# Optimization experiments

Measured on AMD Instinct MI355X. Metric: run time of the kernel, lower is better.

The kernel has to match this reference:

```python
import jax, jax.numpy as jnp
import numpy as np

N_NODES = 50000
N_EDGES = 500000
HEADS = 4
OUT_CH = 64
POS_DIM = 16
IN_CH = 256
DIVERSITY_WEIGHT = 0.1
NEG_SLOPE = 0.2


def setup_inputs() -> dict:
    key = jax.random.key(0)
    k = jax.random.split(key, 6)
    x = jax.random.normal(k[0], (N_NODES, IN_CH + POS_DIM), dtype=jnp.float32)
    # edges with no self-loops by construction (col = row + nonzero offset mod N)
    row = jax.random.randint(k[1], (N_EDGES,), 0, N_NODES)
    off = jax.random.randint(k[2], (N_EDGES,), 1, N_NODES)
    col = (row + off) % N_NODES
    edge_index = jnp.stack([row, col]).astype(jnp.int64)
    lin_w = jax.random.normal(k[3], (HEADS * OUT_CH, IN_CH), dtype=jnp.float32) * (1.0 / np.sqrt(IN_CH))
    att = jax.random.normal(k[4], (1, HEADS, 2 * OUT_CH), dtype=jnp.float32) * 0.1
    pos_att = jax.random.normal(k[5], (1, HEADS, 2 * POS_DIM), dtype=jnp.float32) * 0.1
    bias = jnp.zeros((HEADS * OUT_CH,), dtype=jnp.float32)
    return {"x": x, "edge_index": edge_index, "lin_w": lin_w, "att": att,
            "pos_att": pos_att, "bias": bias}


def _forward(x, edge_index, lin_w, att, pos_att, bias):
    N = x.shape[0]
    H, C = HEADS, OUT_CH
    pos = x[:, -POS_DIM:]              # [N, P]
    content_feat = x[:, :-POS_DIM]     # [N, IN_CH]
    content = (content_feat @ lin_w.T).reshape(N, H, C)  # [N, H, C]

    # add self loops (input edges contain none)
    sl = jnp.arange(N)
    row = jnp.concatenate([edge_index[0], sl])  # [E+N]
    col = jnp.concatenate([edge_index[1], sl])

    # cat([x_i, x_j]) * att summed == per-node split logits, gathered per edge
    a_src = jnp.einsum('nhc,hc->nh', content, att[0, :, :C])   # [N, H]
    a_dst = jnp.einsum('nhc,hc->nh', content, att[0, :, C:])
    p_src = pos @ pos_att[0, :, :POS_DIM].T                    # [N, H]
    p_dst = pos @ pos_att[0, :, POS_DIM:].T

    alpha = a_src[row] + a_dst[col] + p_src[row] + p_dst[col]  # [E+N, H]
    alpha = jax.nn.leaky_relu(alpha, NEG_SLOPE)

    # segment softmax over destination node (row), PyG-style with +1e-16
    amax = jax.ops.segment_max(alpha, row, num_segments=N)
    alpha = jnp.exp(alpha - amax[row])
    denom = jax.ops.segment_sum(alpha, row, num_segments=N)
    alpha = alpha / (denom[row] + 1e-16)

    # attention-head diversity loss: pairwise cosine similarity of alpha columns
    norms = jnp.maximum(jnp.sqrt(jnp.sum(alpha * alpha, axis=0)), 1e-8)  # [H]
    an = alpha / norms
    corr = an.T @ an                                            # [H, H]
    corr = corr * (1.0 - jnp.eye(H, dtype=corr.dtype))          # zero diagonal
    diversity_loss = jnp.mean(corr) * DIVERSITY_WEIGHT

    msgs = content[col] * alpha[:, :, None]                     # [E+N, H, C]
    out = jax.ops.segment_sum(msgs, row, num_segments=N)        # [N, H, C]
    out = out.reshape(N, H * C) + bias
    return out, diversity_loss


def reference(x, edge_index, lin_w, att, pos_att, bias):
    return _forward(x, edge_index, lin_w, att, pos_att, bias)
```

## Files before the change

kernel.cpp:

```cpp
#include <hip/hip_runtime.h>
#include <math.h>

#define NN 50000
#define NE 500000
#define HH 4
#define CC 64
#define HC 256
#define PD 16
#define XD 272
#define NEG 0.2f
#define SB 1024
#define NBLK (NN / 4)

typedef _Float16 half4 __attribute__((ext_vector_type(4)));
typedef _Float16 half8 __attribute__((ext_vector_type(8)));
typedef float floatx4 __attribute__((ext_vector_type(4)));

#define SA 40

__global__ void k_zero(int* counts, int* cursor) {
    int i = blockIdx.x * blockDim.x + threadIdx.x;
    if (i < NN) { counts[i] = 0; cursor[i] = 0; }
}

__global__ __launch_bounds__(256) void k_gemm(const float* __restrict__ x,
                                              const float* __restrict__ w,
                                              _Float16* __restrict__ content) {
    __shared__ _Float16 As[64 * SA];
    __shared__ _Float16 Bs[256 * SA];
    const int tid = threadIdx.x;
    const int wv = tid >> 6, lane = tid & 63;
    const int nb = blockIdx.x * 64;
    const int m16 = lane & 15, q = lane >> 4;

    floatx4 acc[4][4];
#pragma unroll
    for (int mt = 0; mt < 4; mt++)
#pragma unroll
        for (int nt = 0; nt < 4; nt++) acc[mt][nt] = (floatx4){0.f, 0.f, 0.f, 0.f};

    const int arow = tid >> 2, akq = (tid & 3) * 8;
    const int anode = nb + arow;

    for (int kt = 0; kt < 8; kt++) {
        const int k0 = kt * 32;
        __syncthreads();
        {
            float4 f0 = make_float4(0.f, 0.f, 0.f, 0.f), f1 = f0;
            if (anode < NN) {
                f0 = *(const float4*)&x[(size_t)anode * XD + k0 + akq];
                f1 = *(const float4*)&x[(size_t)anode * XD + k0 + akq + 4];
            }
            half8 hv;
            hv[0] = (_Float16)f0.x; hv[1] = (_Float16)f0.y;
            hv[2] = (_Float16)f0.z; hv[3] = (_Float16)f0.w;
            hv[4] = (_Float16)f1.x; hv[5] = (_Float16)f1.y;
            hv[6] = (_Float16)f1.z; hv[7] = (_Float16)f1.w;
            *(half8*)&As[arow * SA + akq] = hv;
        }
        {
            const float* wr = &w[(size_t)tid * 256 + k0];
#pragma unroll
            for (int i = 0; i < 4; i++) {
                float4 f0 = *(const float4*)&wr[i * 8];
                float4 f1 = *(const float4*)&wr[i * 8 + 4];
                half8 hv;
                hv[0] = (_Float16)f0.x; hv[1] = (_Float16)f0.y;
                hv[2] = (_Float16)f0.z; hv[3] = (_Float16)f0.w;
                hv[4] = (_Float16)f1.x; hv[5] = (_Float16)f1.y;
                hv[6] = (_Float16)f1.z; hv[7] = (_Float16)f1.w;
                *(half8*)&Bs[tid * SA + i * 8] = hv;
            }
        }
        __syncthreads();

        half8 af[4], bf[4];
#pragma unroll
        for (int mt = 0; mt < 4; mt++)
            af[mt] = *(half8*)&As[(mt * 16 + m16) * SA + q * 8];
#pragma unroll
        for (int nt = 0; nt < 4; nt++)
            bf[nt] = *(half8*)&Bs[(wv * 64 + nt * 16 + m16) * SA + q * 8];
#pragma unroll
        for (int mt = 0; mt < 4; mt++)
#pragma unroll
            for (int nt = 0; nt < 4; nt++)
                acc[mt][nt] = __builtin_amdgcn_mfma_f32_16x16x32_f16(
                    af[mt], bf[nt], acc[mt][nt], 0, 0, 0);
    }

#pragma unroll
    for (int mt = 0; mt < 4; mt++) {
#pragma unroll
        for (int r = 0; r < 4; r++) {
            int node = nb + mt * 16 + q * 4 + r;
            if (node < NN) {
#pragma unroll
                for (int nt = 0; nt < 4; nt++) {
                    int col = wv * 64 + nt * 16 + m16;
                    content[(size_t)node * 256 + col] = (_Float16)acc[mt][nt][r];
                }
            }
        }
    }
}

__global__ __launch_bounds__(256) void k_score(const _Float16* __restrict__ content,
                                               const float* __restrict__ x,
                                               const float* __restrict__ att,
                                               const float* __restrict__ patt,
                                               float* __restrict__ ssrc,
                                               float* __restrict__ sdst) {
    const int lane = threadIdx.x & 63;
    const int n = blockIdx.x * 4 + (threadIdx.x >> 6);
    const int h = lane >> 4, j = lane & 15;

    half4 v = ((const half4*)content)[(size_t)n * 64 + lane];
    float pv = x[(size_t)n * XD + 256 + j];

    float sa = pv * patt[h * 32 + j];
    float sb = pv * patt[h * 32 + 16 + j];
#pragma unroll
    for (int t = 0; t < 4; t++) {
        float cv = (float)v[t];
        sa += cv * att[h * 128 + j * 4 + t];
        sb += cv * att[h * 128 + 64 + j * 4 + t];
    }
#pragma unroll
    for (int m = 1; m < 16; m <<= 1) {
        sa += __shfl_xor(sa, m, 64);
        sb += __shfl_xor(sb, m, 64);
    }
    if (j == 0) {
        ssrc[n * 4 + h] = sa;
        sdst[n * 4 + h] = sb;
    }
}

__global__ void k_count(const int* __restrict__ row, int* __restrict__ counts) {
    int e = blockIdx.x * blockDim.x + threadIdx.x;
    if (e < NE) atomicAdd(&counts[row[e]], 1);
}

__global__ __launch_bounds__(SB) void k_scan1(const int* __restrict__ counts, int* tmp, int* bsum) {
    __shared__ int s[SB];
    int i = blockIdx.x * SB + threadIdx.x;
    int v = (i < NN) ? counts[i] : 0;
    s[threadIdx.x] = v;
    __syncthreads();
    for (int off = 1; off < SB; off <<= 1) {
        int t = (threadIdx.x >= off) ? s[threadIdx.x - off] : 0;
        __syncthreads();
        s[threadIdx.x] += t;
        __syncthreads();
    }
    if (i < NN) tmp[i] = s[threadIdx.x];
    if (threadIdx.x == SB - 1) bsum[blockIdx.x] = s[SB - 1];
}

__global__ void k_scan2(const int* bsum, int* bcar, int nb) {
    if (threadIdx.x == 0 && blockIdx.x == 0) {
        int c = 0;
        for (int b = 0; b < nb; b++) { bcar[b] = c; c += bsum[b]; }
    }
}

__global__ void k_scan3(const int* tmp, const int* counts, const int* bcar, int* off) {
    int i = blockIdx.x * blockDim.x + threadIdx.x;
    if (i < NN) off[i] = tmp[i] - counts[i] + bcar[i / SB];
}

__global__ void k_scatter(const int* __restrict__ row, const int* __restrict__ col,
                          const int* __restrict__ off, int* __restrict__ cursor,
                          int* __restrict__ sorted) {
    int e = blockIdx.x * blockDim.x + threadIdx.x;
    if (e < NE) {
        int r = row[e];
        int p = off[r] + atomicAdd(&cursor[r], 1);
        sorted[p] = col[e];
    }
}

__global__ __launch_bounds__(256) void k_node(const _Float16* __restrict__ content,
                                              const float* __restrict__ ssrc,
                                              const float* __restrict__ sdst,
                                              const int* __restrict__ counts,
                                              const int* __restrict__ off,
                                              const int* __restrict__ sorted,
                                              const float* __restrict__ bias,
                                              float* __restrict__ out,
                                              float* __restrict__ gpart) {
    __shared__ float gsh[16];
    __shared__ float ash[4][64][4];
    __shared__ int   csh[4][64];
    const int w = threadIdx.x >> 6;
    const int lane = threadIdx.x & 63;
    const int n = blockIdx.x * 4 + w;
    if (threadIdx.x < 16) gsh[threadIdx.x] = 0.f;
    __syncthreads();

    const int cnt = counts[n], base = off[n];
    const int total = cnt + 1;
    const float4 ss = *(const float4*)&ssrc[n * 4];
    const int hsel = lane >> 4;
    const half4* c4 = (const half4*)content;

    float4 acc = make_float4(0.f, 0.f, 0.f, 0.f);
    float g[10];
#pragma unroll
    for (int k = 0; k < 10; k++) g[k] = 0.f;

    if (total <= 64) {
        const int l = lane;
        const bool act = (l < total);
        const int c = (l < cnt) ? sorted[base + l] : n;
        float4 sd = *(const float4*)&sdst[c * 4];
        float r0 = ss.x + sd.x; r0 = r0 > 0.f ? r0 : NEG * r0;
        float r1 = ss.y + sd.y; r1 = r1 > 0.f ? r1 : NEG * r1;
        float r2 = ss.z + sd.z; r2 = r2 > 0.f ? r2 : NEG * r2;
        float r3 = ss.w + sd.w; r3 = r3 > 0.f ? r3 : NEG * r3;
        float m0 = act ? r0 : -1e30f, m1 = act ? r1 : -1e30f;
        float m2 = act ? r2 : -1e30f, m3 = act ? r3 : -1e30f;
#pragma unroll
        for (int s = 1; s < 64; s <<= 1) {
            m0 = fmaxf(m0, __shfl_xor(m0, s));
            m1 = fmaxf(m1, __shfl_xor(m1, s));
            m2 = fmaxf(m2, __shfl_xor(m2, s));
            m3 = fmaxf(m3, __shfl_xor(m3, s));
        }
        float e0 = act ? __expf(r0 - m0) : 0.f;
        float e1 = act ? __expf(r1 - m1) : 0.f;
        float e2 = act ? __expf(r2 - m2) : 0.f;
        float e3 = act ? __expf(r3 - m3) : 0.f;
        float s0 = e0, s1 = e1, s2 = e2, s3 = e3;
#pragma unroll
        for (int s = 1; s < 64; s <<= 1) {
            s0 += __shfl_xor(s0, s); s1 += __shfl_xor(s1, s);
            s2 += __shfl_xor(s2, s); s3 += __shfl_xor(s3, s);
        }
        float a0 = e0 / (s0 + 1e-16f), a1 = e1 / (s1 + 1e-16f);
        float a2 = e2 / (s2 + 1e-16f), a3 = e3 / (s3 + 1e-16f);

        g[0] = a0 * a0; g[1] = a0 * a1; g[2] = a0 * a2; g[3] = a0 * a3;
        g[4] = a1 * a1; g[5] = a1 * a2; g[6] = a1 * a3;
        g[7] = a2 * a2; g[8] = a2 * a3; g[9] = a3 * a3;

        ash[w][l][0] = a0; ash[w][l][1] = a1;
        ash[w][l][2] = a2; ash[w][l][3] = a3;
        csh[w][l] = c;

        const int nit = (total + 7) & ~7;
        for (int e = 0; e < nit; e += 8) {
            int   ci[8];
            float bi[8];
#pragma unroll
            for (int u = 0; u < 8; u++) {
                ci[u] = csh[w][e + u];
                bi[u] = ash[w][e + u][hsel];
            }
            half4 vi[8];
#pragma unroll
            for (int u = 0; u < 8; u++) vi[u] = c4[(size_t)ci[u] * 64 + lane];
#pragma unroll
            for (int u = 0; u < 8; u++) {
                acc.x += bi[u] * (float)vi[u][0];
                acc.y += bi[u] * (float)vi[u][1];
                acc.z += bi[u] * (float)vi[u][2];
                acc.w += bi[u] * (float)vi[u][3];
            }
        }
    } else {
        const int nch = (total + 63) >> 6;
        float m0 = -1e30f, m1 = -1e30f, m2 = -1e30f, m3 = -1e30f;
        for (int ch = 0; ch < nch; ch++) {
            int l = ch * 64 + lane;
            if (l < total) {
                int c = (l < cnt) ? sorted[base + l] : n;
                float4 sd = *(const float4*)&sdst[c * 4];
                float r0 = ss.x + sd.x; r0 = r0 > 0.f ? r0 : NEG * r0;
                float r1 = ss.y + sd.y; r1 = r1 > 0.f ? r1 : NEG * r1;
                float r2 = ss.z + sd.z; r2 = r2 > 0.f ? r2 : NEG * r2;
                float r3 = ss.w + sd.w; r3 = r3 > 0.f ? r3 : NEG * r3;
                m0 = fmaxf(m0, r0); m1 = fmaxf(m1, r1);
                m2 = fmaxf(m2, r2); m3 = fmaxf(m3, r3);
            }
        }
#pragma unroll
        for (int s = 1; s < 64; s <<= 1) {
            m0 = fmaxf(m0, __shfl_xor(m0, s));
            m1 = fmaxf(m1, __shfl_xor(m1, s));
            m2 = fmaxf(m2, __shfl_xor(m2, s));
            m3 = fmaxf(m3, __shfl_xor(m3, s));
        }
        float s0 = 0.f, s1 = 0.f, s2 = 0.f, s3 = 0.f;
        for (int ch = 0; ch < nch; ch++) {
            int l = ch * 64 + lane;
            if (l < total) {
                int c = (l < cnt) ? sorted[base + l] : n;
                float4 sd = *(const float4*)&sdst[c * 4];
                float r0 = ss.x + sd.x; r0 = r0 > 0.f ? r0 : NEG * r0;
                float r1 = ss.y + sd.y; r1 = r1 > 0.f ? r1 : NEG * r1;
                float r2 = ss.z + sd.z; r2 = r2 > 0.f ? r2 : NEG * r2;
                float r3 = ss.w + sd.w; r3 = r3 > 0.f ? r3 : NEG * r3;
                s0 += __expf(r0 - m0); s1 += __expf(r1 - m1);
                s2 += __expf(r2 - m2); s3 += __expf(r3 - m3);
            }
        }
#pragma unroll
        for (int s = 1; s < 64; s <<= 1) {
            s0 += __shfl_xor(s0, s); s1 += __shfl_xor(s1, s);
            s2 += __shfl_xor(s2, s); s3 += __shfl_xor(s3, s);
        }
        const float i0 = 1.f / (s0 + 1e-16f), i1 = 1.f / (s1 + 1e-16f);
        const float i2 = 1.f / (s2 + 1e-16f), i3 = 1.f / (s3 + 1e-16f);

        for (int ch = 0; ch < nch; ch++) {
            int l = ch * 64 + lane;
            int c = n;
            float a0 = 0.f, a1 = 0.f, a2 = 0.f, a3 = 0.f;
            if (l < total) {
                c = (l < cnt) ? sorted[base + l] : n;
                float4 sd = *(const float4*)&sdst[c * 4];
                float r0 = ss.x + sd.x; r0 = r0 > 0.f ? r0 : NEG * r0;
                float r1 = ss.y + sd.y; r1 = r1 > 0.f ? r1 : NEG * r1;
                float r2 = ss.z + sd.z; r2 = r2 > 0.f ? r2 : NEG * r2;
                float r3 = ss.w + sd.w; r3 = r3 > 0.f ? r3 : NEG * r3;
                a0 = __expf(r0 - m0) * i0; a1 = __expf(r1 - m1) * i1;
                a2 = __expf(r2 - m2) * i2; a3 = __expf(r3 - m3) * i3;
            }
            g[0] += a0 * a0; g[1] += a0 * a1; g[2] += a0 * a2; g[3] += a0 * a3;
            g[4] += a1 * a1; g[5] += a1 * a2; g[6] += a1 * a3;
            g[7] += a2 * a2; g[8] += a2 * a3; g[9] += a3 * a3;

            int cc = min(64, total - ch * 64);
            for (int e = 0; e < cc; e++) {
                float b0 = __shfl(a0, e), b1 = __shfl(a1, e);
                float b2 = __shfl(a2, e), b3 = __shfl(a3, e);
                int ce = __shfl(c, e);
                float mya = hsel == 0 ? b0 : hsel == 1 ? b1 : hsel == 2 ? b2 : b3;
                half4 cv = c4[(size_t)ce * 64 + lane];
                acc.x += mya * (float)cv[0]; acc.y += mya * (float)cv[1];
                acc.z += mya * (float)cv[2]; acc.w += mya * (float)cv[3];
            }
        }
    }

    float4 bv = ((const float4*)bias)[lane];
    acc.x += bv.x; acc.y += bv.y; acc.z += bv.z; acc.w += bv.w;
    ((float4*)out)[(size_t)n * 64 + lane] = acc;

#pragma unroll
    for (int s = 1; s < 64; s <<= 1) {
#pragma unroll
        for (int k = 0; k < 10; k++) g[k] += __shfl_xor(g[k], s);
    }
    if (lane == 0) {
#pragma unroll
        for (int k = 0; k < 10; k++) atomicAdd(&gsh[k], g[k]);
    }
    __syncthreads();
    if (threadIdx.x < 10) gpart[(size_t)blockIdx.x * 10 + threadIdx.x] = gsh[threadIdx.x];
}

__global__ __launch_bounds__(1024) void k_final(const float* __restrict__ gpart,
                                                float* __restrict__ out_div) {
    __shared__ float s[1024];
    const int t = threadIdx.x;
    const int k = t & 15, grp = t >> 4;
    float v = 0.f;
    if (k < 10) {
        for (int b = grp; b < NBLK; b += 64) v += gpart[(size_t)b * 10 + k];
    }
    s[t] = v;
    __syncthreads();
    for (int off = 512; off >= 16; off >>= 1) {
        if (t < off) s[t] += s[t + off];
        __syncthreads();
    }
    if (t == 0) {
        float g00 = s[0], g01 = s[1], g02 = s[2], g03 = s[3];
        float g11 = s[4], g12 = s[5], g13 = s[6];
        float g22 = s[7], g23 = s[8], g33 = s[9];
        float n0 = fmaxf(sqrtf(g00), 1e-8f), n1 = fmaxf(sqrtf(g11), 1e-8f);
        float n2 = fmaxf(sqrtf(g22), 1e-8f), n3 = fmaxf(sqrtf(g33), 1e-8f);
        float sum = g01 / (n0 * n1) + g02 / (n0 * n2) + g03 / (n0 * n3) +
                    g12 / (n1 * n2) + g13 / (n1 * n3) + g23 / (n2 * n3);
        sum *= 2.0f;
        out_div[0] = sum / 16.0f * 0.1f;
    }
}

extern "C" void kernel_launch(void* const* d_in, const int* in_sizes, int n_in,
                              void* d_out, int out_size, void* d_ws, size_t ws_size,
                              hipStream_t stream) {
    const float* x    = (const float*)d_in[0];
    const int*   ei   = (const int*)d_in[1];
    const int*   row  = ei;
    const int*   col  = ei + NE;
    const float* w    = (const float*)d_in[2];
    const float* att  = (const float*)d_in[3];
    const float* patt = (const float*)d_in[4];
    const float* bias = (const float*)d_in[5];
    float* out = (float*)d_out;

    char* p = (char*)d_ws;
    _Float16* content = (_Float16*)p; p += (size_t)NN * 256 * 2;
    float* ssrc    = (float*)p; p += (size_t)NN * 4 * 4;
    float* sdst    = (float*)p; p += (size_t)NN * 4 * 4;
    float* gpart   = (float*)p; p += (size_t)NBLK * 10 * 4;
    int* counts    = (int*)p;   p += (size_t)NN * 4;
    int* cursor    = (int*)p;   p += (size_t)NN * 4;
    int* offs      = (int*)p;   p += (size_t)NN * 4;
    int* tmp       = (int*)p;   p += (size_t)NN * 4;
    int* bsum      = (int*)p;   p += 64 * 4;
    int* bcar      = (int*)p;   p += 64 * 4;
    int* sorted    = (int*)p;   p += (size_t)NE * 4;

    k_zero<<<(NN + 255) / 256, 256, 0, stream>>>(counts, cursor);

    k_gemm<<<(NN + 63) / 64, 256, 0, stream>>>(x, w, content);
    k_score<<<NN / 4, 256, 0, stream>>>(content, x, att, patt, ssrc, sdst);

    k_count<<<(NE + 255) / 256, 256, 0, stream>>>(row, counts);
    int nb1 = (NN + SB - 1) / SB;
    k_scan1<<<nb1, SB, 0, stream>>>(counts, tmp, bsum);
    k_scan2<<<1, 64, 0, stream>>>(bsum, bcar, nb1);
    k_scan3<<<(NN + 255) / 256, 256, 0, stream>>>(tmp, counts, bcar, offs);
    k_scatter<<<(NE + 255) / 256, 256, 0, stream>>>(row, col, offs, cursor, sorted);

    k_node<<<NBLK, 256, 0, stream>>>(content, ssrc, sdst, counts, offs, sorted,
                                     bias, out, gpart);
    k_final<<<1, 1024, 0, stream>>>(gpart, out + (size_t)NN * 256);
}
```

Baseline: 337.7 us.

## Prepack weights into MFMA fragments, fuse scoring into GEMM, single-atomic CSR build

A prep kernel converts the weight matrix once into fp16 MFMA fragment order, so the GEMM reads B fragments straight from global memory and no longer stages it through shared memory every k-step. The attention score kernel is folded into the GEMM epilogue, which saves a full re-read of the content array. The CSR build records each edge's slot from the counting atomic, so the placement pass needs no second atomic and no cursor zeroing. The block-carry scan becomes a wave shuffle scan and the aggregation loop unroll grows from 8 to 16. Costs are extra workspace for slot and wfrag, and higher register pressure in the GEMM and aggregation kernels.

```diff
diff --git a/kernel.cpp b/kernel.cpp
--- a/kernel.cpp
+++ b/kernel.cpp
@@ -18,16 +18,25 @@
 
 #define SA 40
 
-__global__ void k_zero(int* counts, int* cursor) {
-    int i = blockIdx.x * blockDim.x + threadIdx.x;
-    if (i < NN) { counts[i] = 0; cursor[i] = 0; }
+__global__ void k_prep(const float* __restrict__ w, _Float16* __restrict__ wfrag,
+                       int* __restrict__ counts) {
+    int idx = blockIdx.x * blockDim.x + threadIdx.x;
+    if (idx < NN) counts[idx] = 0;
+    int j = idx & 7, lane = (idx >> 3) & 63, nt = (idx >> 9) & 3;
+    int wv = (idx >> 11) & 3, kt = idx >> 13;
+    int n = wv * 64 + nt * 16 + (lane & 15);
+    int k = kt * 32 + (lane >> 4) * 8 + j;
+    wfrag[idx] = (_Float16)w[(size_t)n * 256 + k];
 }
 
 __global__ __launch_bounds__(256) void k_gemm(const float* __restrict__ x,
-                                              const float* __restrict__ w,
-                                              _Float16* __restrict__ content) {
+                                              const _Float16* __restrict__ wfrag,
+                                              const float* __restrict__ att,
+                                              const float* __restrict__ patt,
+                                              _Float16* __restrict__ content,
+                                              float* __restrict__ ssrc,
+                                              float* __restrict__ sdst) {
     __shared__ _Float16 As[64 * SA];
-    __shared__ _Float16 Bs[256 * SA];
     const int tid = threadIdx.x;
     const int wv = tid >> 6, lane = tid & 63;
     const int nb = blockIdx.x * 64;
@@ -42,45 +51,30 @@
     const int arow = tid >> 2, akq = (tid & 3) * 8;
     const int anode = nb + arow;
 
+#pragma unroll
     for (int kt = 0; kt < 8; kt++) {
         const int k0 = kt * 32;
         __syncthreads();
-        {
-            float4 f0 = make_float4(0.f, 0.f, 0.f, 0.f), f1 = f0;
-            if (anode < NN) {
-                f0 = *(const float4*)&x[(size_t)anode * XD + k0 + akq];
-                f1 = *(const float4*)&x[(size_t)anode * XD + k0 + akq + 4];
-            }
-            half8 hv;
-            hv[0] = (_Float16)f0.x; hv[1] = (_Float16)f0.y;
-            hv[2] = (_Float16)f0.z; hv[3] = (_Float16)f0.w;
-            hv[4] = (_Float16)f1.x; hv[5] = (_Float16)f1.y;
-            hv[6] = (_Float16)f1.z; hv[7] = (_Float16)f1.w;
-            *(half8*)&As[arow * SA + akq] = hv;
-        }
-        {
-            const float* wr = &w[(size_t)tid * 256 + k0];
-#pragma unroll
-            for (int i = 0; i < 4; i++) {
-                float4 f0 = *(const float4*)&wr[i * 8];
-                float4 f1 = *(const float4*)&wr[i * 8 + 4];
-                half8 hv;
-                hv[0] = (_Float16)f0.x; hv[1] = (_Float16)f0.y;
-                hv[2] = (_Float16)f0.z; hv[3] = (_Float16)f0.w;
-                hv[4] = (_Float16)f1.x; hv[5] = (_Float16)f1.y;
-                hv[6] = (_Float16)f1.z; hv[7] = (_Float16)f1.w;
-                *(half8*)&Bs[tid * SA + i * 8] = hv;
-            }
-        }
+        float4 f0 = make_float4(0.f, 0.f, 0.f, 0.f), f1 = f0;
+        if (anode < NN) {
+            f0 = *(const float4*)&x[(size_t)anode * XD + k0 + akq];
+            f1 = *(const float4*)&x[(size_t)anode * XD + k0 + akq + 4];
+        }
+        half8 hv;
+        hv[0] = (_Float16)f0.x; hv[1] = (_Float16)f0.y;
+        hv[2] = (_Float16)f0.z; hv[3] = (_Float16)f0.w;
+        hv[4] = (_Float16)f1.x; hv[5] = (_Float16)f1.y;
+        hv[6] = (_Float16)f1.z; hv[7] = (_Float16)f1.w;
+        *(half8*)&As[arow * SA + akq] = hv;
         __syncthreads();
 
         half8 af[4], bf[4];
+#pragma unroll
+        for (int nt = 0; nt < 4; nt++)
+            bf[nt] = *(const half8*)&wfrag[((((size_t)kt * 4 + wv) * 4 + nt) * 64 + lane) * 8];
 #pragma unroll
         for (int mt = 0; mt < 4; mt++)
             af[mt] = *(half8*)&As[(mt * 16 + m16) * SA + q * 8];
-#pragma unroll
-        for (int nt = 0; nt < 4; nt++)
-            bf[nt] = *(half8*)&Bs[(wv * 64 + nt * 16 + m16) * SA + q * 8];
 #pragma unroll
         for (int mt = 0; mt < 4; mt++)
 #pragma unroll
@@ -89,57 +83,43 @@
                     af[mt], bf[nt], acc[mt][nt], 0, 0, 0);
     }
 
+    const int h = wv;
 #pragma unroll
     for (int mt = 0; mt < 4; mt++) {
 #pragma unroll
         for (int r = 0; r < 4; r++) {
             int node = nb + mt * 16 + q * 4 + r;
             if (node < NN) {
+                float sa = 0.f, sb = 0.f;
 #pragma unroll
                 for (int nt = 0; nt < 4; nt++) {
-                    int col = wv * 64 + nt * 16 + m16;
-                    content[(size_t)node * 256 + col] = (_Float16)acc[mt][nt][r];
+                    float v = acc[mt][nt][r];
+                    int cih = nt * 16 + m16;
+                    content[(size_t)node * 256 + h * 64 + cih] = (_Float16)v;
+                    sa += v * att[h * 128 + cih];
+                    sb += v * att[h * 128 + 64 + cih];
                 }
-            }
-        }
-    }
-}
-
-__global__ __launch_bounds__(256) void k_score(const _Float16* __restrict__ content,
-                                               const float* __restrict__ x,
-                                               const float* __restrict__ att,
-                                               const float* __restrict__ patt,
-                                               float* __restrict__ ssrc,
-                                               float* __restrict__ sdst) {
-    const int lane = threadIdx.x & 63;
-    const int n = blockIdx.x * 4 + (threadIdx.x >> 6);
-    const int h = lane >> 4, j = lane & 15;
-
-    half4 v = ((const half4*)content)[(size_t)n * 64 + lane];
-    float pv = x[(size_t)n * XD + 256 + j];
-
-    float sa = pv * patt[h * 32 + j];
-    float sb = pv * patt[h * 32 + 16 + j];
-#pragma unroll
-    for (int t = 0; t < 4; t++) {
-        float cv = (float)v[t];
-        sa += cv * att[h * 128 + j * 4 + t];
-        sb += cv * att[h * 128 + 64 + j * 4 + t];
-    }
-#pragma unroll
-    for (int m = 1; m < 16; m <<= 1) {
-        sa += __shfl_xor(sa, m, 64);
-        sb += __shfl_xor(sb, m, 64);
-    }
-    if (j == 0) {
-        ssrc[n * 4 + h] = sa;
-        sdst[n * 4 + h] = sb;
-    }
-}
-
-__global__ void k_count(const int* __restrict__ row, int* __restrict__ counts) {
+                float pv = x[(size_t)node * XD + 256 + m16];
+                sa += pv * patt[h * 32 + m16];
+                sb += pv * patt[h * 32 + 16 + m16];
+#pragma unroll
+                for (int m = 1; m < 16; m <<= 1) {
+                    sa += __shfl_xor(sa, m, 64);
+                    sb += __shfl_xor(sb, m, 64);
+                }
+                if (m16 == 0) {
+                    ssrc[node * 4 + h] = sa;
+                    sdst[node * 4 + h] = sb;
+                }
+            }
+        }
+    }
+}
+
+__global__ void k_count(const int* __restrict__ row, int* __restrict__ counts,
+                        int* __restrict__ slot) {
     int e = blockIdx.x * blockDim.x + threadIdx.x;
-    if (e < NE) atomicAdd(&counts[row[e]], 1);
+    if (e < NE) slot[e] = atomicAdd(&counts[row[e]], 1);
 }
 
 __global__ __launch_bounds__(SB) void k_scan1(const int* __restrict__ counts, int* tmp, int* bsum) {
@@ -158,11 +138,15 @@
     if (threadIdx.x == SB - 1) bsum[blockIdx.x] = s[SB - 1];
 }
 
-__global__ void k_scan2(const int* bsum, int* bcar, int nb) {
-    if (threadIdx.x == 0 && blockIdx.x == 0) {
-        int c = 0;
-        for (int b = 0; b < nb; b++) { bcar[b] = c; c += bsum[b]; }
-    }
+__global__ void k_scan2(const int* __restrict__ bsum, int* __restrict__ bcar, int nb) {
+    int lane = threadIdx.x;
+    int v = (lane < nb) ? bsum[lane] : 0;
+#pragma unroll
+    for (int off = 1; off < 64; off <<= 1) {
+        int t = __shfl_up(v, off);
+        if (lane >= off) v += t;
+    }
+    if (lane < nb) bcar[lane] = v - bsum[lane];
 }
 
 __global__ void k_scan3(const int* tmp, const int* counts, const int* bcar, int* off) {
@@ -170,15 +154,11 @@
     if (i < NN) off[i] = tmp[i] - counts[i] + bcar[i / SB];
 }
 
-__global__ void k_scatter(const int* __restrict__ row, const int* __restrict__ col,
-                          const int* __restrict__ off, int* __restrict__ cursor,
-                          int* __restrict__ sorted) {
+__global__ void k_place(const int* __restrict__ row, const int* __restrict__ col,
+                        const int* __restrict__ offs, const int* __restrict__ slot,
+                        int* __restrict__ sorted) {
     int e = blockIdx.x * blockDim.x + threadIdx.x;
-    if (e < NE) {
-        int r = row[e];
-        int p = off[r] + atomicAdd(&cursor[r], 1);
-        sorted[p] = col[e];
-    }
+    if (e < NE) sorted[offs[row[e]] + slot[e]] = col[e];
 }
 
 __global__ __launch_bounds__(256) void k_node(const _Float16* __restrict__ content,
@@ -249,20 +229,20 @@
         ash[w][l][2] = a2; ash[w][l][3] = a3;
         csh[w][l] = c;
 
-        const int nit = (total + 7) & ~7;
-        for (int e = 0; e < nit; e += 8) {
-            int   ci[8];
-            float bi[8];
-#pragma unroll
-            for (int u = 0; u < 8; u++) {
+        const int nit = (total + 15) & ~15;
+        for (int e = 0; e < nit; e += 16) {
+            int   ci[16];
+            float bi[16];
+#pragma unroll
+            for (int u = 0; u < 16; u++) {
                 ci[u] = csh[w][e + u];
                 bi[u] = ash[w][e + u][hsel];
             }
-            half4 vi[8];
-#pragma unroll
-            for (int u = 0; u < 8; u++) vi[u] = c4[(size_t)ci[u] * 64 + lane];
-#pragma unroll
-            for (int u = 0; u < 8; u++) {
+            half4 vi[16];
+#pragma unroll
+            for (int u = 0; u < 16; u++) vi[u] = c4[(size_t)ci[u] * 64 + lane];
+#pragma unroll
+            for (int u = 0; u < 16; u++) {
                 acc.x += bi[u] * (float)vi[u][0];
                 acc.y += bi[u] * (float)vi[u][1];
                 acc.z += bi[u] * (float)vi[u][2];
@@ -405,28 +385,29 @@
 
     char* p = (char*)d_ws;
     _Float16* content = (_Float16*)p; p += (size_t)NN * 256 * 2;
+    _Float16* wfrag   = (_Float16*)p; p += (size_t)256 * 256 * 2;
     float* ssrc    = (float*)p; p += (size_t)NN * 4 * 4;
     float* sdst    = (float*)p; p += (size_t)NN * 4 * 4;
     float* gpart   = (float*)p; p += (size_t)NBLK * 10 * 4;
     int* counts    = (int*)p;   p += (size_t)NN * 4;
-    int* cursor    = (int*)p;   p += (size_t)NN * 4;
     int* offs      = (int*)p;   p += (size_t)NN * 4;
     int* tmp       = (int*)p;   p += (size_t)NN * 4;
     int* bsum      = (int*)p;   p += 64 * 4;
     int* bcar      = (int*)p;   p += 64 * 4;
+    int* slot      = (int*)p;   p += (size_t)NE * 4;
     int* sorted    = (int*)p;   p += (size_t)NE * 4;
 
-    k_zero<<<(NN + 255) / 256, 256, 0, stream>>>(counts, cursor);
-
-    k_gemm<<<(NN + 63) / 64, 256, 0, stream>>>(x, w, content);
-    k_score<<<NN / 4, 256, 0, stream>>>(content, x, att, patt, ssrc, sdst);
-
-    k_count<<<(NE + 255) / 256, 256, 0, stream>>>(row, counts);
+    k_prep<<<256, 256, 0, stream>>>(w, wfrag, counts);
+
+    k_count<<<(NE + 255) / 256, 256, 0, stream>>>(row, counts, slot);
+
+    k_gemm<<<(NN + 63) / 64, 256, 0, stream>>>(x, wfrag, att, patt, content, ssrc, sdst);
+
     int nb1 = (NN + SB - 1) / SB;
     k_scan1<<<nb1, SB, 0, stream>>>(counts, tmp, bsum);
     k_scan2<<<1, 64, 0, stream>>>(bsum, bcar, nb1);
     k_scan3<<<(NN + 255) / 256, 256, 0, stream>>>(tmp, counts, bcar, offs);
-    k_scatter<<<(NE + 255) / 256, 256, 0, stream>>>(row, col, offs, cursor, sorted);
+    k_place<<<(NE + 255) / 256, 256, 0, stream>>>(row, col, offs, slot, sorted);
 
     k_node<<<NBLK, 256, 0, stream>>>(content, ssrc, sdst, counts, offs, sorted,
                                      bias, out, gpart);
```

Result: faster. 304.4 us (-9.9%).
